# Performance work log

Hardware: AMD Instinct MI355X
Metric: run time of the kernel (lower is better)

The kernel has to match this reference:

```python
import jax, jax.numpy as jnp
import numpy as np
import math

D_MODEL = 1024

def setup_inputs() -> dict:
    key = jax.random.key(0)
    kx, kq, kk, kv = jax.random.split(key, 4)
    scale = 1.0 / math.sqrt(D_MODEL)
    x = jax.random.normal(kx, (4, 2048, D_MODEL), dtype=jnp.float32)
    W_q = jax.random.normal(kq, (D_MODEL, D_MODEL), dtype=jnp.float32) * scale
    W_k = jax.random.normal(kk, (D_MODEL, D_MODEL), dtype=jnp.float32) * scale
    W_v = jax.random.normal(kv, (D_MODEL, D_MODEL), dtype=jnp.float32) * scale
    return {"x": x, "W_q": W_q, "W_k": W_k, "W_v": W_v}

def reference(x, W_q, W_k, W_v):
    # x: (B, C, d)
    B, C, d = x.shape
    Q = x @ W_q  # (B, C, d)
    K = x @ W_k
    V = x @ W_v
    scores = jnp.einsum('bqd,bkd->bqk', Q, K) / jnp.sqrt(jnp.asarray(d, x.dtype))
    causal = jnp.tril(jnp.ones((C, C), dtype=bool))  # (C, C)
    scores = jnp.where(causal, scores, -jnp.inf)
    attn = jax.nn.softmax(scores, axis=-1)
    return jnp.einsum('bqk,bkd->bqd', attn, V)
```

## Files before the change

kernel.cpp:

```cpp
#include <hip/hip_runtime.h>
#include <hip/hip_bf16.h>


typedef __attribute__((ext_vector_type(8))) __bf16 bf16x8;
typedef __attribute__((ext_vector_type(4))) float f32x4;
typedef __attribute__((ext_vector_type(4))) float float4v;
typedef __attribute__((ext_vector_type(4))) unsigned int uint4v;
typedef __attribute__((ext_vector_type(4))) unsigned short ushort4v;

#define GLL16(gp, lp)                                                        \
  __builtin_amdgcn_global_load_lds(                                          \
      (const __attribute__((address_space(1))) void*)(gp),                   \
      (__attribute__((address_space(3))) void*)(lp), 16, 0, 0)

__device__ __forceinline__ unsigned short f2b(float f) {
  union { float f; unsigned u; } v; v.f = f;
  unsigned r = v.u + 0x7FFF + ((v.u >> 16) & 1);
  return (unsigned short)(r >> 16);
}
__device__ __forceinline__ float b2f(unsigned short h) {
  union { unsigned u; float f; } v; v.u = ((unsigned)h) << 16;
  return v.f;
}

__device__ __forceinline__ void store_out(unsigned short* p, float v) { *p = f2b(v); }
__device__ __forceinline__ void store_out(float* p, float v) { *p = v; }

__global__ __launch_bounds__(256) void k_convert(const float* __restrict__ in,
                                                 unsigned short* __restrict__ out, long n) {
  long i = ((long)blockIdx.x * 256 + threadIdx.x) * 4;
  if (i + 3 < n) {
    float4v v = *reinterpret_cast<const float4v*>(in + i);
    ushort4v o;
    o.x = f2b(v.x); o.y = f2b(v.y); o.z = f2b(v.z); o.w = f2b(v.w);
    *reinterpret_cast<ushort4v*>(out + i) = o;
  }
}

__global__ __launch_bounds__(256) void k_transpose_w(const float* __restrict__ in,
                                                     unsigned short* __restrict__ out) {
  __shared__ float t[32][33];
  int tx = threadIdx.x & 31, ty = threadIdx.x >> 5;
  int c0 = blockIdx.x * 32, r0 = blockIdx.y * 32;
  for (int i = ty; i < 32; i += 8)
    t[i][tx] = in[(long)(r0 + i) * 1024 + c0 + tx];
  __syncthreads();
  for (int i = ty; i < 32; i += 8)
    out[(long)(c0 + i) * 1024 + r0 + tx] = f2b(t[tx][i]);
}

__global__ __launch_bounds__(256) void k_transpose_v(const unsigned short* __restrict__ in,
                                                     unsigned short* __restrict__ out,
                                                     int R, int Cc) {
  __shared__ unsigned short t[32][33];
  long base = (long)blockIdx.z * R * Cc;
  int tx = threadIdx.x & 31, ty = threadIdx.x >> 5;
  int c0 = blockIdx.x * 32, r0 = blockIdx.y * 32;
  for (int i = ty; i < 32; i += 8)
    t[i][tx] = in[base + (long)(r0 + i) * Cc + c0 + tx];
  __syncthreads();
  for (int i = ty; i < 32; i += 8)
    out[base + (long)(c0 + i) * R + r0 + tx] = t[tx][i];
}

template <typename OutT, bool CAUSAL_SKIP, bool KCAUSAL>
__global__ __launch_bounds__(256) void k_gemm(const unsigned short* __restrict__ A,
                                              const unsigned short* __restrict__ Bt,
                                              OutT* __restrict__ C,
                                              int M, int N, int K, float scale,
                                              long sA, long sB, long sC) {
  constexpr int BM = 128, BN = 128, BK = 32;
  __shared__ unsigned short As[128 * 32];
  __shared__ unsigned short Bs[128 * 32];
  int bm = blockIdx.x, bn = blockIdx.y;
  if (CAUSAL_SKIP && bn > bm) return;
  long z = blockIdx.z;
  A += z * sA; Bt += z * sB; C += z * sC;

  int tid = threadIdx.x;
  int lane = tid & 63, wave = tid >> 6;
  int wr = (wave >> 1) * 64, wc = (wave & 1) * 64;
  int lr = lane & 15;
  int lk = (lane >> 4) * 8;

  int kend = KCAUSAL ? min(K, (bm + 1) * BM) : K;

  int srow = 32 * wave + (lane >> 2);
  int scol = (lane & 3) * 8;
  const unsigned short* gA = A + (long)(bm * BM + srow) * K + scol;
  const unsigned short* gB = Bt + (long)(bn * BN + srow) * K + scol;
  const long rowK16 = 16L * (long)K;
  unsigned short* lA = &As[(32 * wave) * 32];
  unsigned short* lB = &Bs[(32 * wave) * 32];

  f32x4 acc[4][4] = {};

  for (int k0 = 0; k0 < kend; k0 += BK) {
    GLL16(gA + k0,          lA);
    GLL16(gA + k0 + rowK16, lA + 16 * 32);
    GLL16(gB + k0,          lB);
    GLL16(gB + k0 + rowK16, lB + 16 * 32);
    __syncthreads();

    bf16x8 af[4], bfr[4];
#pragma unroll
    for (int m = 0; m < 4; ++m)
      af[m] = *reinterpret_cast<const bf16x8*>(&As[(wr + m * 16 + lr) * 32 + lk]);
#pragma unroll
    for (int n = 0; n < 4; ++n)
      bfr[n] = *reinterpret_cast<const bf16x8*>(&Bs[(wc + n * 16 + lr) * 32 + lk]);
#pragma unroll
    for (int m = 0; m < 4; ++m)
#pragma unroll
      for (int n = 0; n < 4; ++n)
        acc[m][n] = __builtin_amdgcn_mfma_f32_16x16x32_bf16(af[m], bfr[n], acc[m][n], 0, 0, 0);
    __syncthreads();
  }

  int orow0 = bm * BM + wr + (lane >> 4) * 4;
  int ocol0 = bn * BN + wc + lr;
#pragma unroll
  for (int m = 0; m < 4; ++m)
#pragma unroll
    for (int n = 0; n < 4; ++n)
#pragma unroll
      for (int j = 0; j < 4; ++j) {
        long idx = (long)(orow0 + m * 16 + j) * N + (ocol0 + n * 16);
        store_out(&C[idx], acc[m][n][j] * scale);
      }
}

__global__ __launch_bounds__(256) void k_softmax(unsigned short* __restrict__ S, int Cc) {
  long row = blockIdx.x;
  unsigned short* s = S + row * (long)Cc;
  int r = (int)(row & (Cc - 1));
  int n = r + 1;
  int tid = threadIdx.x;
  int lane = tid & 63, wv = tid >> 6;
  __shared__ float redm[4], reds[4];

  float mx = -3.0e38f;
  for (int c = tid; c < n; c += 256) mx = fmaxf(mx, b2f(s[c]));
#pragma unroll
  for (int o = 32; o > 0; o >>= 1) mx = fmaxf(mx, __shfl_xor(mx, o, 64));
  if (lane == 0) redm[wv] = mx;
  __syncthreads();
  mx = fmaxf(fmaxf(redm[0], redm[1]), fmaxf(redm[2], redm[3]));

  float sum = 0.f;
  for (int c = tid; c < n; c += 256) sum += __expf(b2f(s[c]) - mx);
#pragma unroll
  for (int o = 32; o > 0; o >>= 1) sum += __shfl_xor(sum, o, 64);
  if (lane == 0) reds[wv] = sum;
  __syncthreads();
  sum = reds[0] + reds[1] + reds[2] + reds[3];
  float inv = 1.0f / sum;

  for (int c = tid; c < n; c += 256) s[c] = f2b(__expf(b2f(s[c]) - mx) * inv);
  for (int c = n + tid; c < Cc; c += 256) s[c] = 0;
}

extern "C" void kernel_launch(void* const* d_in, const int* in_sizes, int n_in,
                              void* d_out, int out_size, void* d_ws, size_t ws_size,
                              hipStream_t stream) {
  const int B = 4, C = 2048, D = 1024;
  const long MB = (long)B * C;

  const float* x  = (const float*)d_in[0];
  const float* Wq = (const float*)d_in[1];
  const float* Wk = (const float*)d_in[2];
  const float* Wv = (const float*)d_in[3];
  float* out = (float*)d_out;
  char* ws = (char*)d_ws;

  unsigned short* S   = (unsigned short*)(ws);
  unsigned short* Xb  = (unsigned short*)(ws);
  unsigned short* Wt  = (unsigned short*)(ws + 16777216);
  unsigned short* QKV = (unsigned short*)(ws + 33554432);
  unsigned short* Vt  = (unsigned short*)(ws + 83886080);
  unsigned short* Q  = QKV;
  unsigned short* Kk = QKV + MB * D;
  unsigned short* V  = QKV + 2L * MB * D;

  k_convert<<<8192, 256, 0, stream>>>(x, Xb, MB * D);

  dim3 gw(32, 32);
  k_transpose_w<<<gw, 256, 0, stream>>>(Wq, Wt);
  k_transpose_w<<<gw, 256, 0, stream>>>(Wk, Wt + 1048576);
  k_transpose_w<<<gw, 256, 0, stream>>>(Wv, Wt + 2097152);

  k_gemm<unsigned short, false, false><<<dim3(64, 8, 3), 256, 0, stream>>>(
      Xb, Wt, QKV, (int)MB, D, D, 1.0f, 0L, (long)D * D, MB * D);

  k_transpose_v<<<dim3(32, 64, 4), 256, 0, stream>>>(V, Vt, C, D);

  k_gemm<unsigned short, true, false><<<dim3(16, 16, 4), 256, 0, stream>>>(
      Q, Kk, S, C, C, D, 1.0f / 32.0f, (long)C * D, (long)C * D, (long)C * C);

  k_softmax<<<B * C, 256, 0, stream>>>(S, C);

  k_gemm<float, false, true><<<dim3(16, 8, 4), 256, 0, stream>>>(
      S, Vt, out, C, D, C, 1.0f, (long)C * C, (long)D * C, (long)C * D);
}
```

Before: 314.1 us.

## Replace GEMM with 256x256 tile, 8-wave double-buffered pipelined kernel

Replaces the 128x128 BK=32 single-buffered GEMM with a 256x256 tile kernel using 512 threads, 128-wide K steps split into two 64-wide double-buffered LDS stages, XOR-swizzled LDS layout, and an interleaved schedule of global-to-LDS loads, LDS reads and MFMA quadrants separated by barriers and priority hints. It aims to hide global load latency, cut LDS bank conflicts and raise arithmetic intensity per tile. Larger tiles reduce the block count (e.g. 384 blocks for QKV, fewer for causal GEMMs), which can hurt load balance and coarsen causal skipping. The 128 KB of LDS per block also limits occupancy.

```diff
diff --git a/kernel.cpp b/kernel.cpp
--- a/kernel.cpp
+++ b/kernel.cpp
@@ -5,7 +5,6 @@
 typedef __attribute__((ext_vector_type(8))) __bf16 bf16x8;
 typedef __attribute__((ext_vector_type(4))) float f32x4;
 typedef __attribute__((ext_vector_type(4))) float float4v;
-typedef __attribute__((ext_vector_type(4))) unsigned int uint4v;
 typedef __attribute__((ext_vector_type(4))) unsigned short ushort4v;
 
 #define GLL16(gp, lp)                                                        \
@@ -13,6 +12,13 @@
       (const __attribute__((address_space(1))) void*)(gp),                   \
       (__attribute__((address_space(3))) void*)(lp), 16, 0, 0)
 
+#define BAR()  __builtin_amdgcn_s_barrier()
+#define SB0()  __builtin_amdgcn_sched_barrier(0)
+#define WLG0() asm volatile("s_waitcnt lgkmcnt(0)" ::: "memory")
+#define WVM4() asm volatile("s_waitcnt vmcnt(4)" ::: "memory")
+#define WVM0() asm volatile("s_waitcnt vmcnt(0)" ::: "memory")
+#define PRIO(n) __builtin_amdgcn_s_setprio(n)
+
 __device__ __forceinline__ unsigned short f2b(float f) {
   union { float f; unsigned u; } v; v.f = f;
   unsigned r = v.u + 0x7FFF + ((v.u >> 16) & 1);
@@ -22,7 +28,6 @@
   union { unsigned u; float f; } v; v.u = ((unsigned)h) << 16;
   return v.f;
 }
-
 __device__ __forceinline__ void store_out(unsigned short* p, float v) { *p = f2b(v); }
 __device__ __forceinline__ void store_out(float* p, float v) { *p = v; }
 
@@ -63,70 +68,135 @@
     out[base + (long)(c0 + i) * R + r0 + tx] = t[tx][i];
 }
 
+
+#define RDA(buf, half)                                                        \
+  _Pragma("unroll") for (int m_ = 0; m_ < 4; ++m_)                            \
+  _Pragma("unroll") for (int ks_ = 0; ks_ < 2; ++ks_)                         \
+    af[m_][ks_] = *reinterpret_cast<const bf16x8*>(                           \
+        (buf) + (arb + (half) * 4 + m_) * 1024 + ks_ * 512 + foff);
+
+#define RDB(buf, half, BF)                                                    \
+  _Pragma("unroll") for (int n_ = 0; n_ < 2; ++n_)                            \
+  _Pragma("unroll") for (int ks_ = 0; ks_ < 2; ++ks_)                         \
+    BF[n_][ks_] = *reinterpret_cast<const bf16x8*>(                           \
+        (buf) + (brb + (half) * 2 + n_) * 1024 + ks_ * 512 + foff);
+
+#define QUAD(mh, nh, BF)                                                      \
+  _Pragma("unroll") for (int m_ = 0; m_ < 4; ++m_)                            \
+  _Pragma("unroll") for (int n_ = 0; n_ < 2; ++n_)                            \
+  _Pragma("unroll") for (int ks_ = 0; ks_ < 2; ++ks_)                         \
+    acc[(mh) * 4 + m_][(nh) * 2 + n_] =                                       \
+        __builtin_amdgcn_mfma_f32_16x16x32_bf16(                              \
+            af[m_][ks_], BF[n_][ks_], acc[(mh) * 4 + m_][(nh) * 2 + n_], 0, 0, 0);
+
+#define STGA(buf, h, k0)                                                      \
+  GLL16(gA + (long)(128 * (h)) * K + (k0),      (buf) + (16 * (h) + wave) * 512); \
+  GLL16(gA + (long)(128 * (h) + 64) * K + (k0), (buf) + (16 * (h) + 8 + wave) * 512);
+
+#define STGB(buf, h, k0)                                                      \
+  GLL16(gB + (long)(128 * (h)) * K + (k0),      (buf) + (16 * (h) + wave) * 512); \
+  GLL16(gB + (long)(128 * (h) + 64) * K + (k0), (buf) + (16 * (h) + 8 + wave) * 512);
+
 template <typename OutT, bool CAUSAL_SKIP, bool KCAUSAL>
-__global__ __launch_bounds__(256) void k_gemm(const unsigned short* __restrict__ A,
-                                              const unsigned short* __restrict__ Bt,
-                                              OutT* __restrict__ C,
-                                              int M, int N, int K, float scale,
-                                              long sA, long sB, long sC) {
-  constexpr int BM = 128, BN = 128, BK = 32;
-  __shared__ unsigned short As[128 * 32];
-  __shared__ unsigned short Bs[128 * 32];
-  int bm = blockIdx.x, bn = blockIdx.y;
+__global__ __launch_bounds__(512, 2) void k_gemm256(
+    const unsigned short* __restrict__ A, const unsigned short* __restrict__ Bt,
+    OutT* __restrict__ C, int M, int N, int K, float scale,
+    long sA, long sB, long sC) {
+  constexpr int BM = 256;
+  __shared__ __align__(16) unsigned short lds[65536];
+  unsigned short* const lA0 = lds;
+  unsigned short* const lA1 = lds + 16384;
+  unsigned short* const lB0 = lds + 32768;
+  unsigned short* const lB1 = lds + 49152;
+
+  const int bm = blockIdx.x, bn = blockIdx.y;
   if (CAUSAL_SKIP && bn > bm) return;
-  long z = blockIdx.z;
+  const long z = blockIdx.z;
   A += z * sA; Bt += z * sB; C += z * sC;
 
-  int tid = threadIdx.x;
-  int lane = tid & 63, wave = tid >> 6;
-  int wr = (wave >> 1) * 64, wc = (wave & 1) * 64;
-  int lr = lane & 15;
-  int lk = (lane >> 4) * 8;
-
-  int kend = KCAUSAL ? min(K, (bm + 1) * BM) : K;
-
-  int srow = 32 * wave + (lane >> 2);
-  int scol = (lane & 3) * 8;
-  const unsigned short* gA = A + (long)(bm * BM + srow) * K + scol;
-  const unsigned short* gB = Bt + (long)(bn * BN + srow) * K + scol;
-  const long rowK16 = 16L * (long)K;
-  unsigned short* lA = &As[(32 * wave) * 32];
-  unsigned short* lB = &Bs[(32 * wave) * 32];
-
-  f32x4 acc[4][4] = {};
-
-  for (int k0 = 0; k0 < kend; k0 += BK) {
-    GLL16(gA + k0,          lA);
-    GLL16(gA + k0 + rowK16, lA + 16 * 32);
-    GLL16(gB + k0,          lB);
-    GLL16(gB + k0 + rowK16, lB + 16 * 32);
-    __syncthreads();
-
-    bf16x8 af[4], bfr[4];
-#pragma unroll
-    for (int m = 0; m < 4; ++m)
-      af[m] = *reinterpret_cast<const bf16x8*>(&As[(wr + m * 16 + lr) * 32 + lk]);
-#pragma unroll
-    for (int n = 0; n < 4; ++n)
-      bfr[n] = *reinterpret_cast<const bf16x8*>(&Bs[(wc + n * 16 + lr) * 32 + lk]);
-#pragma unroll
-    for (int m = 0; m < 4; ++m)
-#pragma unroll
-      for (int n = 0; n < 4; ++n)
-        acc[m][n] = __builtin_amdgcn_mfma_f32_16x16x32_bf16(af[m], bfr[n], acc[m][n], 0, 0, 0);
-    __syncthreads();
+  const int tid = threadIdx.x;
+  const int lane = tid & 63, wave = tid >> 6;
+  const int row0 = bm * BM, col0 = bn * 256;
+
+  const int kend = KCAUSAL ? min(K, (bm + 1) * BM) : K;
+  const int niter = kend >> 7;
+
+  const int scol = ((lane & 3) * 8) ^ ((lane & 32) ? 16 : 0);
+  const int srowi = (wave >> 1) * 16 + (lane >> 2);
+  const int scolw = (wave & 1) * 32 + scol;
+  const unsigned short* gA = A + (long)(row0 + srowi) * K + scolw;
+  const unsigned short* gB = Bt + (long)(col0 + srowi) * K + scolw;
+
+  const int foff = ((lane & 15) * 32 + (lane >> 4) * 8) ^ ((lane & 8) ? 16 : 0);
+  const int arb = 8 * (wave >> 2);
+  const int brb = 4 * (wave & 3);
+
+  bf16x8 af[4][2], bf0[2][2], bf1[2][2];
+  f32x4 acc[8][4] = {};
+
+  STGA(lA0, 0, 0); STGA(lA0, 1, 0);
+  STGB(lB0, 0, 0); STGB(lB0, 1, 0);
+  STGB(lB1, 0, 64); STGA(lA1, 0, 64);
+  WVM4();
+  BAR(); SB0();
+
+  for (int j = 0; j < niter; ++j) {
+    const bool last = (j == niter - 1);
+    const int kb = j * 128;
+    RDA(lA0, 0); RDB(lB0, 0, bf0);
+    STGA(lA1, 1, kb + 64);
+    BAR(); WLG0(); SB0();
+    PRIO(1); QUAD(0, 0, bf0); PRIO(0);
+    BAR(); SB0();
+    RDB(lB0, 1, bf1);
+    STGB(lB1, 1, kb + 64);
+    BAR(); WLG0(); SB0();
+    PRIO(1); QUAD(0, 1, bf1); PRIO(0);
+    BAR(); SB0();
+    RDA(lA0, 1);
+    if (!last) { STGB(lB0, 0, kb + 128); }
+    BAR(); WLG0(); SB0();
+    PRIO(1); QUAD(1, 1, bf1); PRIO(0);
+    BAR(); SB0();
+    if (!last) { STGA(lA0, 0, kb + 128); }
+    BAR();
+    if (!last) { WVM4(); } else { WVM0(); }
+    SB0();
+    PRIO(1); QUAD(1, 0, bf0); PRIO(0);
+    BAR(); SB0();
+    RDA(lA1, 0); RDB(lB1, 0, bf0);
+    if (!last) { STGA(lA0, 1, kb + 128); }
+    BAR(); WLG0(); SB0();
+    PRIO(1); QUAD(0, 0, bf0); PRIO(0);
+    BAR(); SB0();
+    RDB(lB1, 1, bf1);
+    if (!last) { STGB(lB0, 1, kb + 128); }
+    BAR(); WLG0(); SB0();
+    PRIO(1); QUAD(0, 1, bf1); PRIO(0);
+    BAR(); SB0();
+    RDA(lA1, 1);
+    if (!last) { STGB(lB1, 0, kb + 192); }
+    BAR(); WLG0(); SB0();
+    PRIO(1); QUAD(1, 1, bf1); PRIO(0);
+    BAR(); SB0();
+    if (!last) { STGA(lA1, 0, kb + 192); }
+    BAR();
+    if (!last) { WVM4(); }
+    SB0();
+    PRIO(1); QUAD(1, 0, bf0); PRIO(0);
+    BAR(); SB0();
   }
 
-  int orow0 = bm * BM + wr + (lane >> 4) * 4;
-  int ocol0 = bn * BN + wc + lr;
-#pragma unroll
-  for (int m = 0; m < 4; ++m)
-#pragma unroll
-    for (int n = 0; n < 4; ++n)
-#pragma unroll
-      for (int j = 0; j < 4; ++j) {
-        long idx = (long)(orow0 + m * 16 + j) * N + (ocol0 + n * 16);
-        store_out(&C[idx], acc[m][n][j] * scale);
+  const int or0 = row0 + (wave >> 2) * 128 + (lane >> 4) * 4;
+  const int oc0 = col0 + (wave & 3) * 64 + (lane & 15);
+#pragma unroll
+  for (int mm = 0; mm < 8; ++mm)
+#pragma unroll
+    for (int nn = 0; nn < 4; ++nn)
+#pragma unroll
+      for (int jj = 0; jj < 4; ++jj) {
+        long idx = (long)(or0 + mm * 16 + jj) * N + (oc0 + nn * 16);
+        store_out(&C[idx], acc[mm][nn][jj] * scale);
       }
 }
 
@@ -189,16 +259,16 @@
   k_transpose_w<<<gw, 256, 0, stream>>>(Wk, Wt + 1048576);
   k_transpose_w<<<gw, 256, 0, stream>>>(Wv, Wt + 2097152);
 
-  k_gemm<unsigned short, false, false><<<dim3(64, 8, 3), 256, 0, stream>>>(
+  k_gemm256<unsigned short, false, false><<<dim3(32, 4, 3), 512, 0, stream>>>(
       Xb, Wt, QKV, (int)MB, D, D, 1.0f, 0L, (long)D * D, MB * D);
 
   k_transpose_v<<<dim3(32, 64, 4), 256, 0, stream>>>(V, Vt, C, D);
 
-  k_gemm<unsigned short, true, false><<<dim3(16, 16, 4), 256, 0, stream>>>(
+  k_gemm256<unsigned short, true, false><<<dim3(8, 8, 4), 512, 0, stream>>>(
       Q, Kk, S, C, C, D, 1.0f / 32.0f, (long)C * D, (long)C * D, (long)C * C);
 
   k_softmax<<<B * C, 256, 0, stream>>>(S, C);
 
-  k_gemm<float, false, true><<<dim3(16, 8, 4), 256, 0, stream>>>(
+  k_gemm256<float, false, true><<<dim3(8, 4, 4), 512, 0, stream>>>(
       S, Vt, out, C, D, C, 1.0f, (long)C * C, (long)D * C, (long)C * D);
 }
```

After: 277.7 us. 1.13x faster.
